# Kernel optimization log

Hardware: AMD Instinct MI355X
Metric: run time of the kernel (lower is better)

Reference implementation:

```python
import jax, jax.numpy as jnp
import numpy as np

N_NODE = 4095
D_EMB = 32
D_MODEL = 64
NHEADS = 8
ALPHA = 1.0
B = N_NODE + 1  # batch must equal n_node+1 (see einsum 'nm,tmd->tnd')
T = 32


def setup_inputs() -> dict:
    key = jax.random.key(0)
    ks = jax.random.split(key, 16)
    f32 = jnp.float32
    inp = {
        "q": jax.random.normal(ks[0], (B, T, D_MODEL), f32),
        "k": jax.random.normal(ks[1], (B, T, D_MODEL), f32),
        "v": jax.random.normal(ks[2], (B, T, D_MODEL), f32),
        # learned parameters (torch init is randn; scaled for numeric stability)
        "emb": jax.random.normal(ks[3], (N_NODE + 1, D_EMB), f32) * 0.05,
        "We": jax.random.normal(ks[4], (D_EMB, D_MODEL, D_MODEL), f32) * 0.05,
        "be": jax.random.normal(ks[5], (D_EMB, D_MODEL), f32) * 0.05,
        "Wq": jax.random.normal(ks[6], (D_MODEL, D_MODEL), f32) * 0.05,
        "bq": jax.random.normal(ks[7], (D_MODEL,), f32) * 0.05,
        "Wk": jax.random.normal(ks[8], (D_MODEL, D_MODEL), f32) * 0.05,
        "bk": jax.random.normal(ks[9], (D_MODEL,), f32) * 0.05,
        "Wv": jax.random.normal(ks[10], (D_MODEL, D_MODEL), f32) * 0.05,
        "bv": jax.random.normal(ks[11], (D_MODEL,), f32) * 0.05,
        "Wo": jax.random.normal(ks[12], (D_MODEL, D_MODEL), f32) * 0.05,
        "bo": jax.random.normal(ks[13], (D_MODEL,), f32) * 0.05,
    }
    return inp


def _elu(x, alpha):
    return jnp.where(x > 0, x, alpha * (jnp.exp(x) - 1.0))


def _split_heads(x, h):
    # torch.cat(torch.split(x, D//h, dim=-1), dim=0): [B,T,D] -> [h*B,T,D/h]
    b, t, d = x.shape
    return jnp.moveaxis(x.reshape(b, t, h, d // h), 2, 0).reshape(h * b, t, d // h)


def _merge_heads(x, b, h):
    # torch.cat(torch.split(x, B, dim=0), dim=-1): [h*B,T,D/h] -> [B,T,D]
    hb, t, dh = x.shape
    return jnp.moveaxis(x.reshape(h, b, t, dh), 0, 2).reshape(b, t, h * dh)


def reference(q, k, v, emb, We, be, Wq, bq, Wk, bk, Wv, bv, Wo, bo):
    Bq, Tq, D = q.shape
    h = NHEADS
    scale = (D // h) ** 0.5

    # linear projections (torch Linear: x @ W.T + b)
    q = q @ Wq.T + bq
    k = k @ Wk.T + bk
    v = v @ Wv.T + bv

    # adjacency: sum over d_emb of pairwise diff == s_i - s_j (same math, no [N,N,E] tensor)
    s = jnp.sum(emb, axis=-1)  # [N+1]
    sim = s[:, None] - s[None, :]  # [N+1, N+1]
    A = jax.nn.softmax(_elu(sim, ALPHA), axis=-1) + jnp.eye(Bq, dtype=q.dtype)

    # updateQ: adjacency-weighted diffusion + per-node weight matrices
    qt = jnp.transpose(q, (1, 0, 2))  # [T, N, D]
    W = jnp.einsum('ne,eio->nio', emb, We)  # [N, D, D]
    b = emb @ be  # [N, D]
    q_ = jnp.einsum('nm,tmd->tnd', A, qt)  # diffusion
    q_ = jnp.einsum('tnd,ndo->tno', q_, W) + b  # per-node matmul
    q = jnp.transpose(q_, (1, 0, 2))  # [N, T, D]

    # manual multi-head attention via split/cat
    qh = _split_heads(q, h)
    kh = _split_heads(k, h)
    vh = _split_heads(v, h)
    attn = jax.nn.softmax(jnp.einsum('btd,bsd->bts', qh, kh) / scale, axis=-1)
    out = jnp.einsum('bts,bsd->btd', attn, vh)
    out = _merge_heads(out, Bq, h)
    return out @ Wo.T + bo
```

## Files before the change

kernel.cpp:

```cpp
#include <hip/hip_runtime.h>
#include <hip/hip_bf16.h>

constexpr int NN  = 4096;
constexpr int DE  = 32;
constexpr int TD  = 2048;

typedef __attribute__((ext_vector_type(8))) short short8;
typedef __attribute__((ext_vector_type(4))) float f32x4;

#define MFMA16(a, b, c) __builtin_amdgcn_mfma_f32_16x16x32_bf16(a, b, c, 0, 0, 0)

__device__ inline ushort f2b(float x) {
    __hip_bfloat16 h = __float2bfloat16(x);
    union { __hip_bfloat16 h; ushort u; } c; c.h = h;
    return c.u;
}

__device__ inline float b2f(ushort u) {
    union { unsigned u; float f; } c; c.u = ((unsigned)u) << 16;
    return c.f;
}

__device__ inline short8 pack8(float4 a, float4 b) {
    short8 v;
    v[0] = (short)f2b(a.x); v[1] = (short)f2b(a.y); v[2] = (short)f2b(a.z); v[3] = (short)f2b(a.w);
    v[4] = (short)f2b(b.x); v[5] = (short)f2b(b.y); v[6] = (short)f2b(b.z); v[7] = (short)f2b(b.w);
    return v;
}

__device__ inline short8 pack8v(f32x4 a, f32x4 b) {
    short8 v;
    v[0] = (short)f2b(a[0]); v[1] = (short)f2b(a[1]); v[2] = (short)f2b(a[2]); v[3] = (short)f2b(a[3]);
    v[4] = (short)f2b(b[0]); v[5] = (short)f2b(b[1]); v[6] = (short)f2b(b[2]); v[7] = (short)f2b(b[3]);
    return v;
}

__device__ __forceinline__ short8 as_s8(f32x4 v) {
    union { f32x4 f; short8 s; } u; u.f = v; return u.s;
}

template<int OFF>
__device__ __forceinline__ f32x4 gl16(unsigned long long addr) {
    f32x4 d;
    asm volatile("global_load_dwordx4 %0, %1, off offset:%c2"
                 : "=v"(d) : "v"(addr), "n"(OFF) : "memory");
    return d;
}

template<int OFF>
__device__ __forceinline__ float gl4(unsigned long long addr) {
    float d;
    asm volatile("global_load_dword %0, %1, off offset:%c2"
                 : "=v"(d) : "v"(addr), "n"(OFF) : "memory");
    return d;
}

#define WAITV(N) asm volatile("s_waitcnt vmcnt(" #N ")" ::: "memory"); \
                 __builtin_amdgcn_sched_barrier(0)

__global__ __launch_bounds__(256) void k_prep(const float* __restrict__ emb,
                                              const float* __restrict__ We,
                                              const float* __restrict__ be,
                                              const float* __restrict__ Wk,
                                              const float* __restrict__ Wv,
                                              const float* __restrict__ Wo,
                                              float* __restrict__ s_g,
                                              ushort* __restrict__ embbf,
                                              ushort* __restrict__ WeTT,
                                              ushort* __restrict__ Wkbf,
                                              ushort* __restrict__ Wvbf,
                                              ushort* __restrict__ Wobf,
                                              float* __restrict__ bn) {
    int id = blockIdx.x, tid = threadIdx.x;
    if (id < 16) {
        int n = id * 256 + tid;
        const float4* e4 = (const float4*)(emb + n * DE);
        float s = 0.f;
#pragma unroll
        for (int i = 0; i < DE / 4; ++i) { float4 v = e4[i]; s += v.x + v.y + v.z + v.w; }
        s_g[n] = s;
    } else if (id < 144) {
        int g4 = (id - 16) * 256 + tid;
        float4 v = *(const float4*)&emb[(size_t)g4 * 4];
        ushort4 o; o.x = f2b(v.x); o.y = f2b(v.y); o.z = f2b(v.z); o.w = f2b(v.w);
        *(ushort4*)&embbf[(size_t)g4 * 4] = o;
    } else if (id < 176) {
        int e = id - 144;
#pragma unroll
        for (int u = 0; u < 4; ++u) {
            int idx0 = tid * 16 + u * 4;
            float4 v = *(const float4*)&We[(size_t)e * 4096 + idx0];
            float vv[4] = {v.x, v.y, v.z, v.w};
#pragma unroll
            for (int i = 0; i < 4; ++i) {
                int idx = idx0 + i;
                int o = idx & 63, d = idx >> 6;
                WeTT[(size_t)(o * 64 + d) * 32 + e] = f2b(vv[i]);
            }
        }
    } else if (id < 224) {
        int id5 = id - 176;
        int which = id5 >> 4, gid = (id5 & 15) * 256 + tid;
        const float* src = which == 0 ? Wk : (which == 1 ? Wv : Wo);
        ushort* dst = which == 0 ? Wkbf : (which == 1 ? Wvbf : Wobf);
        dst[gid] = f2b(src[gid]);
    } else {
        int gid = (id - 224) * 256 + tid;
        int n = gid >> 6, o = gid & 63;
        float acc = 0.f;
#pragma unroll
        for (int e = 0; e < DE; ++e) acc += emb[n * DE + e] * be[e * 64 + o];
        bn[gid] = acc;
    }
}

__global__ __launch_bounds__(256) void k_pr(const float* __restrict__ X,
                                            const float* __restrict__ W,
                                            const float* __restrict__ bias,
                                            ushort* __restrict__ Y,
                                            const float* __restrict__ s_g,
                                            int* __restrict__ perm) {
    __shared__ float ss[NN];
    int id = blockIdx.x, tid = threadIdx.x;
    if (id < 512) {
        int lane = tid & 63, wid = tid >> 6;
        int r0 = id * 256 + wid * 64;
        int l15 = lane & 15, kb = lane >> 4;
        f32x4 acc[4][4] = {};
#pragma unroll
        for (int kk = 0; kk < 2; ++kk) {
            short8 af[4], bf[4];
#pragma unroll
            for (int f = 0; f < 4; ++f) {
                const float* ap = X + (size_t)(r0 + f * 16 + l15) * 64 + kk * 32 + kb * 8;
                af[f] = pack8(*(const float4*)ap, *(const float4*)(ap + 4));
                const float* bp = W + (size_t)(f * 16 + l15) * 64 + kk * 32 + kb * 8;
                bf[f] = pack8(*(const float4*)bp, *(const float4*)(bp + 4));
            }
#pragma unroll
            for (int i = 0; i < 4; ++i)
#pragma unroll
                for (int j = 0; j < 4; ++j)
                    acc[i][j] = MFMA16(af[i], bf[j], acc[i][j]);
        }
        float bcol[4];
#pragma unroll
        for (int j = 0; j < 4; ++j) bcol[j] = bias[j * 16 + l15];
#pragma unroll
        for (int i = 0; i < 4; ++i)
#pragma unroll
            for (int j = 0; j < 4; ++j)
#pragma unroll
                for (int r = 0; r < 4; ++r)
                    Y[(size_t)(r0 + i * 16 + kb * 4 + r) * 64 + j * 16 + l15] =
                        f2b(acc[i][j][r] + bcol[j]);
    } else {
        for (int i = tid; i < NN; i += 256) ss[i] = s_g[i];
        __syncthreads();
        int g = tid >> 5, l = tid & 31;
        int n = (id - 512) * 8 + g;
        float sn = ss[n];
        int cnt = 0;
        for (int j2 = 0; j2 < 128; ++j2) {
            int m = j2 * 32 + l;
            float sm = ss[m];
            cnt += (sm < sn) || (sm == sn && m < n);
        }
        for (int off = 16; off; off >>= 1) cnt += __shfl_down(cnt, off, 32);
        if (l == 0) perm[cnt] = n;
    }
}

__global__ __launch_bounds__(256) void k_csum(const ushort* __restrict__ qp,
                                              const float* __restrict__ s_g,
                                              const int* __restrict__ perm,
                                              float* __restrict__ Cj,
                                              float* __restrict__ Cb) {
    __shared__ int ns[64];
    __shared__ float bs[64];
    int bx = blockIdx.x, by = blockIdx.y, tid = threadIdx.x;
    if (tid < 64) {
        int n = perm[bx * 64 + tid];
        ns[tid] = n;
        bs[tid] = __expf(-s_g[n]);
    }
    __syncthreads();
    int j = by * 256 + tid;
    float run[8] = {};
    for (int ii = 0; ii < 64; ++ii) {
        float qv = b2f(qp[(size_t)ns[ii] * 2048 + j]);
        float b = bs[ii], t = qv;
#pragma unroll
        for (int k2 = 0; k2 < 8; ++k2) { run[k2] += t; t *= b; }
    }
    float* cp = Cj + ((size_t)bx * 2048 + j) * 8;
    *(float4*)cp       = make_float4(run[0], run[1], run[2], run[3]);
    *(float4*)(cp + 4) = make_float4(run[4], run[5], run[6], run[7]);
    if (by == 0 && tid < 64) {
        float b = bs[tid], bk = 1.f;
#pragma unroll
        for (int k2 = 0; k2 < 8; ++k2) {
            float v = bk;
            for (int off = 32; off; off >>= 1) v += __shfl_down(v, off, 64);
            if (tid == 0) Cb[bx * 8 + k2] = v;
            bk *= b;
        }
    }
}

__global__ __launch_bounds__(256) void k_pre(const float* __restrict__ Cj,
                                             float* __restrict__ PRE,
                                             const float* __restrict__ Cb,
                                             float* __restrict__ CbPre) {
    __shared__ float sCb[512];
    int tid = threadIdx.x;
    if (blockIdx.x < 64) {
        int gid = blockIdx.x * 256 + tid;
        float run = 0.f;
#pragma unroll 8
        for (int c = 0; c < 64; ++c) {
            PRE[(size_t)c * 16384 + gid] = run;
            run += Cj[(size_t)c * 16384 + gid];
        }
        PRE[(size_t)64 * 16384 + gid] = run;
    } else {
        sCb[tid] = Cb[tid];
        sCb[tid + 256] = Cb[tid + 256];
        __syncthreads();
        if (tid < 8) {
            float run = 0.f;
            for (int c = 0; c < 64; ++c) {
                CbPre[c * 8 + tid] = run;
                run += sCb[c * 8 + tid];
            }
            CbPre[512 + tid] = run;
        }
    }
}

__global__ __launch_bounds__(256) void k_combw(const ushort* __restrict__ qp,
                                               const float* __restrict__ s_g,
                                               const int* __restrict__ perm,
                                               const float* __restrict__ PRE,
                                               const float* __restrict__ CbPre,
                                               ushort* __restrict__ qdifb,
                                               const ushort* __restrict__ embbf,
                                               const ushort* __restrict__ WeTT,
                                               ushort* __restrict__ WnT) {
    __shared__ int ns[64];
    __shared__ float sa[64], sb[64];
    int id = blockIdx.x, tid = threadIdx.x;
    if (id < 512) {
        int bx = id & 63, by = id >> 6;
        if (tid < 64) {
            int n = perm[bx * 64 + tid];
            ns[tid] = n;
            float s = s_g[n];
            sa[tid] = __expf(s);
            sb[tid] = __expf(-s);
        }
        __syncthreads();
        int j = by * 256 + tid;
        float T[8], pre[8];
        {
            const float* pp = PRE + (size_t)bx * 16384 + (size_t)j * 8;
            float4 u0 = *(const float4*)pp, u1 = *(const float4*)(pp + 4);
            pre[0] = u0.x; pre[1] = u0.y; pre[2] = u0.z; pre[3] = u0.w;
            pre[4] = u1.x; pre[5] = u1.y; pre[6] = u1.z; pre[7] = u1.w;
            const float* tp = PRE + (size_t)64 * 16384 + (size_t)j * 8;
            float4 t0 = *(const float4*)tp, t1 = *(const float4*)(tp + 4);
            T[0] = t0.x; T[1] = t0.y; T[2] = t0.z; T[3] = t0.w;
            T[4] = t1.x; T[5] = t1.y; T[6] = t1.z; T[7] = t1.w;
        }
        float TB[8], preb[8];
        {
            float4 v0 = *(const float4*)&CbPre[bx * 8], v1 = *(const float4*)&CbPre[bx * 8 + 4];
            preb[0] = v0.x; preb[1] = v0.y; preb[2] = v0.z; preb[3] = v0.w;
            preb[4] = v1.x; preb[5] = v1.y; preb[6] = v1.z; preb[7] = v1.w;
            float4 t0 = *(const float4*)&CbPre[512], t1 = *(const float4*)&CbPre[516];
            TB[0] = t0.x; TB[1] = t0.y; TB[2] = t0.z; TB[3] = t0.w;
            TB[4] = t1.x; TB[5] = t1.y; TB[6] = t1.z; TB[7] = t1.w;
        }
#pragma unroll 2
        for (int ii = 0; ii < 64; ++ii) {
            int n = ns[ii];
            float a = sa[ii], b = sb[ii];
            float g0 = 0.36787944117144233f;
            float g1 = g0 * a;
            float g2 = g1 * a * 0.5f;
            float g3 = g2 * a * (1.f / 3.f);
            float g4 = g3 * a * 0.25f;
            float g5 = g4 * a * 0.2f;
            float g6 = g5 * a * (1.f / 6.f);
            float g7 = g6 * a * (1.f / 7.f);
            float Z = a * preb[1]
                    + g0 * (TB[0] - preb[0]) + g1 * (TB[1] - preb[1])
                    + g2 * (TB[2] - preb[2]) + g3 * (TB[3] - preb[3])
                    + g4 * (TB[4] - preb[4]) + g5 * (TB[5] - preb[5])
                    + g6 * (TB[6] - preb[6]) + g7 * (TB[7] - preb[7]);
            float izv = 1.f / Z;
            float qv = b2f(qp[(size_t)n * 2048 + j]);
            float ss2 = g0 * (T[0] - pre[0]) + g1 * (T[1] - pre[1])
                      + g2 * (T[2] - pre[2]) + g3 * (T[3] - pre[3])
                      + g4 * (T[4] - pre[4]) + g5 * (T[5] - pre[5])
                      + g6 * (T[6] - pre[6]) + g7 * (T[7] - pre[7]);
            float outv = (a * pre[1] + ss2) * izv + qv;
            qdifb[(size_t)n * 2048 + j] = f2b(outv);
            float bk = 1.f;
#pragma unroll
            for (int k2 = 0; k2 < 8; ++k2) { pre[k2] += bk * qv; preb[k2] += bk; bk *= b; }
        }
    } else {
        int w2 = id - 512;
        int lane = tid & 63, wid = tid >> 6;
        int n0  = (w2 & 31) * 128 + (wid >> 1) * 64;
        int od0 = (w2 >> 5) * 128 + (wid & 1) * 64;
        int l15 = lane & 15, kb = lane >> 4;
        short8 af[4], bf[4];
#pragma unroll
        for (int f = 0; f < 4; ++f) {
            af[f] = *(const short8*)(embbf + (size_t)(n0 + f * 16 + l15) * 32 + kb * 8);
            bf[f] = *(const short8*)(WeTT + (size_t)(od0 + f * 16 + l15) * 32 + kb * 8);
        }
        f32x4 acc[4][4] = {};
#pragma unroll
        for (int i = 0; i < 4; ++i)
#pragma unroll
            for (int j = 0; j < 4; ++j)
                acc[i][j] = MFMA16(af[i], bf[j], acc[i][j]);
#pragma unroll
        for (int i = 0; i < 4; ++i)
#pragma unroll
            for (int j = 0; j < 4; ++j)
#pragma unroll
                for (int r = 0; r < 4; ++r)
                    WnT[(size_t)(n0 + i * 16 + kb * 4 + r) * 4096 + od0 + j * 16 + l15] =
                        f2b(acc[i][j][r]);
    }
}

__global__ __launch_bounds__(256, 2) void k_fused(const float* __restrict__ kin,
                                                  const float* __restrict__ vin,
                                                  const ushort* __restrict__ qdifb,
                                                  const ushort* __restrict__ WnT,
                                                  const float* __restrict__ bn,
                                                  const ushort* __restrict__ Wkbf,
                                                  const float* __restrict__ bk,
                                                  const ushort* __restrict__ Wvbf,
                                                  const float* __restrict__ bv,
                                                  const ushort* __restrict__ Wobf,
                                                  const float* __restrict__ bo,
                                                  float* __restrict__ out) {
    __shared__ ushort Kb[2176];
    __shared__ ushort Qb[2176];
    __shared__ ushort Vb[2560];
    __shared__ ushort Pb[4][1280];
    __shared__ ushort attb[2304];
    int tid = threadIdx.x, lane = tid & 63, w = tid >> 6;
    int b = blockIdx.x;
    int l15 = lane & 15, g = lane >> 4;
    int hh_w = l15 >> 3, d1_w = l15 & 7;
    const float SCALE = 0.35355339059327373f;
    short8 zfrag = {};

    f32x4 wx0, wx1, wx2, wx3, wx4, wx5, wx6, wx7;
    f32x4 x0, x1, x2, x3, x4, x5, x6, x7;
    float bxc0, bxc1, bxc2, bxc3;
    f32x4 q0v, q1v, q2v, q3v;
    f32x4 wn0, wn1, wn2, wn3;
    float bnc0, bnc1;
    f32x4 wo0, wo1; float boc;

    if (w < 2) {
        const float*  xin = w ? vin : kin;
        const ushort* Wx  = w ? Wvbf : Wkbf;
        const float*  bx_ = w ? bv : bk;
        unsigned long long bxA = (unsigned long long)(bx_ + l15);
        unsigned long long wxA = (unsigned long long)((const char*)Wx + l15 * 128 + g * 16 + 3072);
        unsigned long long xaA = (unsigned long long)(xin + (size_t)b * TD + (8 + l15) * 64 + g * 8);
        bxc0 = gl4<0>(bxA); bxc1 = gl4<64>(bxA); bxc2 = gl4<128>(bxA); bxc3 = gl4<192>(bxA);
        wx0 = gl16<-3072>(wxA); wx1 = gl16<-3008>(wxA);
        wx2 = gl16<-1024>(wxA); wx3 = gl16< -960>(wxA);
        wx4 = gl16< 1024>(wxA); wx5 = gl16< 1088>(wxA);
        wx6 = gl16< 3072>(wxA); wx7 = gl16< 3136>(wxA);
        x0 = gl16<-2048>(xaA); x1 = gl16<-2032>(xaA);
        x2 = gl16<-1920>(xaA); x3 = gl16<-1904>(xaA);
        x4 = gl16< 2048>(xaA); x5 = gl16< 2064>(xaA);
        x6 = gl16< 2176>(xaA); x7 = gl16< 2192>(xaA);
    } else {
        int wq = w - 2;
        unsigned long long qaA = (unsigned long long)(qdifb + (size_t)b * TD + (8 + l15) * 64 + g * 8);
        unsigned long long wnA = (unsigned long long)((const char*)(WnT + (size_t)b * 4096)
                                                      + ((size_t)(wq * 32 + l15)) * 128 + g * 16);
        unsigned long long bnA = (unsigned long long)(bn + (size_t)b * 64 + wq * 32 + l15);
        q0v = gl16<-1024>(qaA); q1v = gl16<-960>(qaA);
        q2v = gl16< 1024>(qaA); q3v = gl16<1088>(qaA);
        wn0 = gl16<0>(wnA); wn1 = gl16<64>(wnA);
        wn2 = gl16<2048>(wnA); wn3 = gl16<2112>(wnA);
        bnc0 = gl4<0>(bnA); bnc1 = gl4<64>(bnA);
    }
    {
        unsigned long long woA = (unsigned long long)((const char*)Wobf
                                                      + ((size_t)(w * 16 + l15)) * 128 + g * 16);
        unsigned long long boA = (unsigned long long)(bo + w * 16 + l15);
        wo0 = gl16<0>(woA); wo1 = gl16<64>(woA);
        boc = gl4<0>(boA);
    }

    if (w < 2) {
        WAITV(3);
        short8 xaf[2][2], wxf[4][2];
        xaf[0][0] = pack8v(x0, x1); xaf[1][0] = pack8v(x2, x3);
        xaf[0][1] = pack8v(x4, x5); xaf[1][1] = pack8v(x6, x7);
        wxf[0][0] = as_s8(wx0); wxf[0][1] = as_s8(wx1);
        wxf[1][0] = as_s8(wx2); wxf[1][1] = as_s8(wx3);
        wxf[2][0] = as_s8(wx4); wxf[2][1] = as_s8(wx5);
        wxf[3][0] = as_s8(wx6); wxf[3][1] = as_s8(wx7);
        float bxc[4] = {bxc0, bxc1, bxc2, bxc3};
#pragma unroll
        for (int j = 0; j < 4; ++j) {
            f32x4 ax[2] = {};
#pragma unroll
            for (int kk = 0; kk < 2; ++kk)
#pragma unroll
                for (int ti = 0; ti < 2; ++ti)
                    ax[ti] = MFMA16(xaf[kk][ti], wxf[j][kk], ax[ti]);
            if (w == 0) {
#pragma unroll
                for (int ti = 0; ti < 2; ++ti)
#pragma unroll
                    for (int r = 0; r < 4; ++r) {
                        int s = ti * 16 + g * 4 + r;
                        Kb[(j * 2 + hh_w) * 272 + s * 8 + d1_w] = f2b(ax[ti][r] + bxc[j]);
                    }
            } else {
#pragma unroll
                for (int ti = 0; ti < 2; ++ti)
#pragma unroll
                    for (int r = 0; r < 4; r += 2) {
                        int s = ti * 16 + g * 4 + r;
                        ushort2 p; p.x = f2b(ax[ti][r] + bxc[j]); p.y = f2b(ax[ti][r + 1] + bxc[j]);
                        *(ushort2*)&Vb[(j * 2 + hh_w) * 320 + d1_w * 40 + s] = p;
                    }
            }
        }
    } else {
        int wq = w - 2;
        WAITV(3);
        short8 qaf[2][2], wnf[2][2];
        qaf[0][0] = as_s8(q0v); qaf[1][0] = as_s8(q1v);
        qaf[0][1] = as_s8(q2v); qaf[1][1] = as_s8(q3v);
        wnf[0][0] = as_s8(wn0); wnf[0][1] = as_s8(wn1);
        wnf[1][0] = as_s8(wn2); wnf[1][1] = as_s8(wn3);
        float bnc[2] = {bnc0, bnc1};
#pragma unroll
        for (int jj = 0; jj < 2; ++jj) {
            int j = 2 * wq + jj;
            f32x4 aq[2] = {};
#pragma unroll
            for (int kk = 0; kk < 2; ++kk)
#pragma unroll
                for (int ti = 0; ti < 2; ++ti)
                    aq[ti] = MFMA16(qaf[kk][ti], wnf[jj][kk], aq[ti]);
#pragma unroll
            for (int ti = 0; ti < 2; ++ti)
#pragma unroll
                for (int r = 0; r < 4; ++r) {
                    int s = ti * 16 + g * 4 + r;
                    Qb[(j * 2 + hh_w) * 272 + s * 8 + d1_w] = f2b(aq[ti][r] + bnc[jj]);
                }
        }
    }
    __syncthreads();

#pragma unroll
    for (int hh = 0; hh < 2; ++hh) {
        int h = 2 * w + hh;
        short8 kf[2], qf[2];
#pragma unroll
        for (int si = 0; si < 2; ++si)
            kf[si] = (lane < 16) ? *(const short8*)&Kb[h * 272 + (si * 16 + l15) * 8] : zfrag;
#pragma unroll
        for (int ti = 0; ti < 2; ++ti)
            qf[ti] = (lane < 16) ? *(const short8*)&Qb[h * 272 + (ti * 16 + l15) * 8] : zfrag;
        f32x4 sc[2][2];
#pragma unroll
        for (int si = 0; si < 2; ++si)
#pragma unroll
            for (int ti = 0; ti < 2; ++ti)
                sc[si][ti] = MFMA16(kf[si], qf[ti], f32x4{});
#pragma unroll
        for (int ti = 0; ti < 2; ++ti) {
            float e0[4], e1[4], sm = 0.f;
#pragma unroll
            for (int r = 0; r < 4; ++r) {
                e0[r] = __expf(sc[0][ti][r] * SCALE);
                e1[r] = __expf(sc[1][ti][r] * SCALE);
                sm += e0[r] + e1[r];
            }
            sm += __shfl_xor(sm, 16);
            sm += __shfl_xor(sm, 32);
            float inv = 1.f / sm;
            int t = ti * 16 + l15;
            unsigned p00 = (unsigned)f2b(e0[0] * inv) | ((unsigned)f2b(e0[1] * inv) << 16);
            unsigned p01 = (unsigned)f2b(e0[2] * inv) | ((unsigned)f2b(e0[3] * inv) << 16);
            unsigned p10 = (unsigned)f2b(e1[0] * inv) | ((unsigned)f2b(e1[1] * inv) << 16);
            unsigned p11 = (unsigned)f2b(e1[2] * inv) | ((unsigned)f2b(e1[3] * inv) << 16);
            *(unsigned*)&Pb[w][t * 40 + g * 4]          = p00;
            *(unsigned*)&Pb[w][t * 40 + g * 4 + 2]      = p01;
            *(unsigned*)&Pb[w][t * 40 + 16 + g * 4]     = p10;
            *(unsigned*)&Pb[w][t * 40 + 16 + g * 4 + 2] = p11;
        }
        short8 vf = *(const short8*)&Vb[h * 320 + (l15 & 7) * 40 + g * 8];
#pragma unroll
        for (int ti = 0; ti < 2; ++ti) {
            short8 af = *(const short8*)&Pb[w][(ti * 16 + l15) * 40 + g * 8];
            f32x4 pv = MFMA16(af, vf, f32x4{});
            if (l15 < 8) {
#pragma unroll
                for (int r = 0; r < 4; ++r)
                    attb[(ti * 16 + g * 4 + r) * 72 + h * 8 + l15] = f2b(pv[r]);
            }
        }
    }
    __syncthreads();

    WAITV(0);
    {
        short8 wof[2];
        wof[0] = as_s8(wo0); wof[1] = as_s8(wo1);
        short8 aof[2][2];
#pragma unroll
        for (int kk = 0; kk < 2; ++kk)
#pragma unroll
            for (int ti = 0; ti < 2; ++ti)
                aof[kk][ti] = *(const short8*)&attb[(ti * 16 + l15) * 72 + kk * 32 + g * 8];
        f32x4 co[2] = {};
#pragma unroll
        for (int kk = 0; kk < 2; ++kk)
#pragma unroll
            for (int ti = 0; ti < 2; ++ti)
                co[ti] = MFMA16(aof[kk][ti], wof[kk], co[ti]);
#pragma unroll
        for (int ti = 0; ti < 2; ++ti)
#pragma unroll
            for (int r = 0; r < 4; ++r)
                out[(size_t)b * TD + (ti * 16 + g * 4 + r) * 64 + w * 16 + l15] =
                    co[ti][r] + boc;
    }
}

extern "C" void kernel_launch(void* const* d_in, const int* in_sizes, int n_in,
                              void* d_out, int out_size, void* d_ws, size_t ws_size,
                              hipStream_t stream) {
    const float* q   = (const float*)d_in[0];
    const float* k   = (const float*)d_in[1];
    const float* v   = (const float*)d_in[2];
    const float* emb = (const float*)d_in[3];
    const float* We  = (const float*)d_in[4];
    const float* be  = (const float*)d_in[5];
    const float* Wq  = (const float*)d_in[6];
    const float* bq  = (const float*)d_in[7];
    const float* Wk  = (const float*)d_in[8];
    const float* bk  = (const float*)d_in[9];
    const float* Wv  = (const float*)d_in[10];
    const float* bv  = (const float*)d_in[11];
    const float* Wo  = (const float*)d_in[12];
    const float* bo  = (const float*)d_in[13];

    float* ws = (float*)d_ws;
    ushort* qp    = (ushort*)ws;
    ushort* WnT   = (ushort*)(ws + 4194304);
    ushort* qdifb = (ushort*)(ws + 12582912);
    float*  Cj    = ws + 16777216;
    float*  bn    = ws + 17825792;
    float*  s_g   = ws + 18087936;
    int*    perm  = (int*)(ws + 18092032);
    float*  Cb    = ws + 18096128;
    ushort* embbf = (ushort*)(ws + 18096640);
    ushort* WeTT  = (ushort*)(ws + 18162176);
    ushort* Wkbf  = (ushort*)(ws + 18227712);
    ushort* Wvbf  = (ushort*)(ws + 18229760);
    ushort* Wobf  = (ushort*)(ws + 18231808);
    float*  PRE   = ws + 18233856;
    float*  CbPre = ws + 19298816;
    float*  outp  = (float*)d_out;

    k_prep <<<1248, 256, 0, stream>>>(emb, We, be, Wk, Wv, Wo,
                                      s_g, embbf, WeTT, Wkbf, Wvbf, Wobf, bn);
    k_pr   <<<1024, 256, 0, stream>>>(q, Wq, bq, qp, s_g, perm);
    k_csum <<<dim3(64, 8), 256, 0, stream>>>(qp, s_g, perm, Cj, Cb);
    k_pre  <<<65, 256, 0, stream>>>(Cj, PRE, Cb, CbPre);
    k_combw<<<1536, 256, 0, stream>>>(qp, s_g, perm, PRE, CbPre, qdifb,
                                      embbf, WeTT, WnT);
    k_fused<<<4096, 256, 0, stream>>>(k, v, qdifb, WnT, bn,
                                      Wkbf, bk, Wvbf, bv, Wobf, bo, outp);
}
```

Before: 107.0 us.

## Process two nodes per block in fused attention kernel, prefetching second node's inputs

```diff
diff --git a/kernel.cpp b/kernel.cpp
--- a/kernel.cpp
+++ b/kernel.cpp
@@ -357,7 +357,7 @@
     __shared__ ushort Pb[4][1280];
     __shared__ ushort attb[2304];
     int tid = threadIdx.x, lane = tid & 63, w = tid >> 6;
-    int b = blockIdx.x;
+    int b0 = blockIdx.x * 2;
     int l15 = lane & 15, g = lane >> 4;
     int hh_w = l15 >> 3, d1_w = l15 & 7;
     const float SCALE = 0.35355339059327373f;
@@ -365,10 +365,11 @@
 
     f32x4 wx0, wx1, wx2, wx3, wx4, wx5, wx6, wx7;
     f32x4 x0, x1, x2, x3, x4, x5, x6, x7;
+    f32x4 y0, y1, y2, y3, y4, y5, y6, y7;
     float bxc0, bxc1, bxc2, bxc3;
-    f32x4 q0v, q1v, q2v, q3v;
-    f32x4 wn0, wn1, wn2, wn3;
-    float bnc0, bnc1;
+    f32x4 q0v, q1v, q2v, q3v, wn0, wn1, wn2, wn3;
+    f32x4 r0v, r1v, r2v, r3v, um0, um1, um2, um3;
+    float bn0c0, bn0c1, bn1c0, bn1c1;
     f32x4 wo0, wo1; float boc;
 
     if (w < 2) {
@@ -377,7 +378,8 @@
         const float*  bx_ = w ? bv : bk;
         unsigned long long bxA = (unsigned long long)(bx_ + l15);
         unsigned long long wxA = (unsigned long long)((const char*)Wx + l15 * 128 + g * 16 + 3072);
-        unsigned long long xaA = (unsigned long long)(xin + (size_t)b * TD + (8 + l15) * 64 + g * 8);
+        unsigned long long xaA = (unsigned long long)(xin + (size_t)b0 * TD + (8 + l15) * 64 + g * 8);
+        unsigned long long yaA = (unsigned long long)(xin + (size_t)(b0 + 1) * TD + (8 + l15) * 64 + g * 8);
         bxc0 = gl4<0>(bxA); bxc1 = gl4<64>(bxA); bxc2 = gl4<128>(bxA); bxc3 = gl4<192>(bxA);
         wx0 = gl16<-3072>(wxA); wx1 = gl16<-3008>(wxA);
         wx2 = gl16<-1024>(wxA); wx3 = gl16< -960>(wxA);
@@ -387,31 +389,49 @@
         x2 = gl16<-1920>(xaA); x3 = gl16<-1904>(xaA);
         x4 = gl16< 2048>(xaA); x5 = gl16< 2064>(xaA);
         x6 = gl16< 2176>(xaA); x7 = gl16< 2192>(xaA);
+        {
+            unsigned long long woA = (unsigned long long)((const char*)Wobf
+                                                          + ((size_t)(w * 16 + l15)) * 128 + g * 16);
+            unsigned long long boA = (unsigned long long)(bo + w * 16 + l15);
+            wo0 = gl16<0>(woA); wo1 = gl16<64>(woA);
+            boc = gl4<0>(boA);
+        }
+        y0 = gl16<-2048>(yaA); y1 = gl16<-2032>(yaA);
+        y2 = gl16<-1920>(yaA); y3 = gl16<-1904>(yaA);
+        y4 = gl16< 2048>(yaA); y5 = gl16< 2064>(yaA);
+        y6 = gl16< 2176>(yaA); y7 = gl16< 2192>(yaA);
     } else {
         int wq = w - 2;
-        unsigned long long qaA = (unsigned long long)(qdifb + (size_t)b * TD + (8 + l15) * 64 + g * 8);
-        unsigned long long wnA = (unsigned long long)((const char*)(WnT + (size_t)b * 4096)
+        unsigned long long qaA = (unsigned long long)(qdifb + (size_t)b0 * TD + (8 + l15) * 64 + g * 8);
+        unsigned long long wnA = (unsigned long long)((const char*)(WnT + (size_t)b0 * 4096)
                                                       + ((size_t)(wq * 32 + l15)) * 128 + g * 16);
-        unsigned long long bnA = (unsigned long long)(bn + (size_t)b * 64 + wq * 32 + l15);
+        unsigned long long bnA = (unsigned long long)(bn + (size_t)b0 * 64 + wq * 32 + l15);
+        unsigned long long qbA = (unsigned long long)(qdifb + (size_t)(b0 + 1) * TD + (8 + l15) * 64 + g * 8);
+        unsigned long long wmA = (unsigned long long)((const char*)(WnT + (size_t)(b0 + 1) * 4096)
+                                                      + ((size_t)(wq * 32 + l15)) * 128 + g * 16);
+        unsigned long long bmA = (unsigned long long)(bn + (size_t)(b0 + 1) * 64 + wq * 32 + l15);
         q0v = gl16<-1024>(qaA); q1v = gl16<-960>(qaA);
         q2v = gl16< 1024>(qaA); q3v = gl16<1088>(qaA);
         wn0 = gl16<0>(wnA); wn1 = gl16<64>(wnA);
         wn2 = gl16<2048>(wnA); wn3 = gl16<2112>(wnA);
-        bnc0 = gl4<0>(bnA); bnc1 = gl4<64>(bnA);
-    }
-    {
-        unsigned long long woA = (unsigned long long)((const char*)Wobf
-                                                      + ((size_t)(w * 16 + l15)) * 128 + g * 16);
-        unsigned long long boA = (unsigned long long)(bo + w * 16 + l15);
-        wo0 = gl16<0>(woA); wo1 = gl16<64>(woA);
-        boc = gl4<0>(boA);
-    }
-
-    if (w < 2) {
-        WAITV(3);
-        short8 xaf[2][2], wxf[4][2];
-        xaf[0][0] = pack8v(x0, x1); xaf[1][0] = pack8v(x2, x3);
-        xaf[0][1] = pack8v(x4, x5); xaf[1][1] = pack8v(x6, x7);
+        bn0c0 = gl4<0>(bnA); bn0c1 = gl4<64>(bnA);
+        {
+            unsigned long long woA = (unsigned long long)((const char*)Wobf
+                                                          + ((size_t)(w * 16 + l15)) * 128 + g * 16);
+            unsigned long long boA = (unsigned long long)(bo + w * 16 + l15);
+            wo0 = gl16<0>(woA); wo1 = gl16<64>(woA);
+            boc = gl4<0>(boA);
+        }
+        r0v = gl16<-1024>(qbA); r1v = gl16<-960>(qbA);
+        r2v = gl16< 1024>(qbA); r3v = gl16<1088>(qbA);
+        um0 = gl16<0>(wmA); um1 = gl16<64>(wmA);
+        um2 = gl16<2048>(wmA); um3 = gl16<2112>(wmA);
+        bn1c0 = gl4<0>(bmA); bn1c1 = gl4<64>(bmA);
+    }
+
+    auto kvProj = [&](short8 xaf00, short8 xaf10, short8 xaf01, short8 xaf11) {
+        short8 xaf[2][2] = {{xaf00, xaf01}, {xaf10, xaf11}};
+        short8 wxf[4][2];
         wxf[0][0] = as_s8(wx0); wxf[0][1] = as_s8(wx1);
         wxf[1][0] = as_s8(wx2); wxf[1][1] = as_s8(wx3);
         wxf[2][0] = as_s8(wx4); wxf[2][1] = as_s8(wx5);
@@ -444,15 +464,14 @@
                     }
             }
         }
-    } else {
+    };
+    auto qProj = [&](short8 qa00, short8 qa10, short8 qa01, short8 qa11,
+                     short8 wf00, short8 wf01, short8 wf10, short8 wf11,
+                     float bc0, float bc1) {
+        short8 qaf[2][2] = {{qa00, qa01}, {qa10, qa11}};
+        short8 wnf[2][2] = {{wf00, wf01}, {wf10, wf11}};
+        float bnc[2] = {bc0, bc1};
         int wq = w - 2;
-        WAITV(3);
-        short8 qaf[2][2], wnf[2][2];
-        qaf[0][0] = as_s8(q0v); qaf[1][0] = as_s8(q1v);
-        qaf[0][1] = as_s8(q2v); qaf[1][1] = as_s8(q3v);
-        wnf[0][0] = as_s8(wn0); wnf[0][1] = as_s8(wn1);
-        wnf[1][0] = as_s8(wn2); wnf[1][1] = as_s8(wn3);
-        float bnc[2] = {bnc0, bnc1};
 #pragma unroll
         for (int jj = 0; jj < 2; ++jj) {
             int j = 2 * wq + jj;
@@ -470,63 +489,60 @@
                     Qb[(j * 2 + hh_w) * 272 + s * 8 + d1_w] = f2b(aq[ti][r] + bnc[jj]);
                 }
         }
-    }
-    __syncthreads();
-
-#pragma unroll
-    for (int hh = 0; hh < 2; ++hh) {
-        int h = 2 * w + hh;
-        short8 kf[2], qf[2];
-#pragma unroll
-        for (int si = 0; si < 2; ++si)
-            kf[si] = (lane < 16) ? *(const short8*)&Kb[h * 272 + (si * 16 + l15) * 8] : zfrag;
-#pragma unroll
-        for (int ti = 0; ti < 2; ++ti)
-            qf[ti] = (lane < 16) ? *(const short8*)&Qb[h * 272 + (ti * 16 + l15) * 8] : zfrag;
-        f32x4 sc[2][2];
-#pragma unroll
-        for (int si = 0; si < 2; ++si)
+    };
+    auto attn = [&]() {
+#pragma unroll
+        for (int hh = 0; hh < 2; ++hh) {
+            int h = 2 * w + hh;
+            short8 kf[2], qf[2];
+#pragma unroll
+            for (int si = 0; si < 2; ++si)
+                kf[si] = (lane < 16) ? *(const short8*)&Kb[h * 272 + (si * 16 + l15) * 8] : zfrag;
 #pragma unroll
             for (int ti = 0; ti < 2; ++ti)
-                sc[si][ti] = MFMA16(kf[si], qf[ti], f32x4{});
-#pragma unroll
-        for (int ti = 0; ti < 2; ++ti) {
-            float e0[4], e1[4], sm = 0.f;
-#pragma unroll
-            for (int r = 0; r < 4; ++r) {
-                e0[r] = __expf(sc[0][ti][r] * SCALE);
-                e1[r] = __expf(sc[1][ti][r] * SCALE);
-                sm += e0[r] + e1[r];
+                qf[ti] = (lane < 16) ? *(const short8*)&Qb[h * 272 + (ti * 16 + l15) * 8] : zfrag;
+            f32x4 sc[2][2];
+#pragma unroll
+            for (int si = 0; si < 2; ++si)
+#pragma unroll
+                for (int ti = 0; ti < 2; ++ti)
+                    sc[si][ti] = MFMA16(kf[si], qf[ti], f32x4{});
+#pragma unroll
+            for (int ti = 0; ti < 2; ++ti) {
+                float e0[4], e1[4], sm = 0.f;
+#pragma unroll
+                for (int r = 0; r < 4; ++r) {
+                    e0[r] = __expf(sc[0][ti][r] * SCALE);
+                    e1[r] = __expf(sc[1][ti][r] * SCALE);
+                    sm += e0[r] + e1[r];
+                }
+                sm += __shfl_xor(sm, 16);
+                sm += __shfl_xor(sm, 32);
+                float inv = 1.f / sm;
+                int t = ti * 16 + l15;
+                unsigned p00 = (unsigned)f2b(e0[0] * inv) | ((unsigned)f2b(e0[1] * inv) << 16);
+                unsigned p01 = (unsigned)f2b(e0[2] * inv) | ((unsigned)f2b(e0[3] * inv) << 16);
+                unsigned p10 = (unsigned)f2b(e1[0] * inv) | ((unsigned)f2b(e1[1] * inv) << 16);
+                unsigned p11 = (unsigned)f2b(e1[2] * inv) | ((unsigned)f2b(e1[3] * inv) << 16);
+                *(unsigned*)&Pb[w][t * 40 + g * 4]          = p00;
+                *(unsigned*)&Pb[w][t * 40 + g * 4 + 2]      = p01;
+                *(unsigned*)&Pb[w][t * 40 + 16 + g * 4]     = p10;
+                *(unsigned*)&Pb[w][t * 40 + 16 + g * 4 + 2] = p11;
             }
-            sm += __shfl_xor(sm, 16);
-            sm += __shfl_xor(sm, 32);
-            float inv = 1.f / sm;
-            int t = ti * 16 + l15;
-            unsigned p00 = (unsigned)f2b(e0[0] * inv) | ((unsigned)f2b(e0[1] * inv) << 16);
-            unsigned p01 = (unsigned)f2b(e0[2] * inv) | ((unsigned)f2b(e0[3] * inv) << 16);
-            unsigned p10 = (unsigned)f2b(e1[0] * inv) | ((unsigned)f2b(e1[1] * inv) << 16);
-            unsigned p11 = (unsigned)f2b(e1[2] * inv) | ((unsigned)f2b(e1[3] * inv) << 16);
-            *(unsigned*)&Pb[w][t * 40 + g * 4]          = p00;
-            *(unsigned*)&Pb[w][t * 40 + g * 4 + 2]      = p01;
-            *(unsigned*)&Pb[w][t * 40 + 16 + g * 4]     = p10;
-            *(unsigned*)&Pb[w][t * 40 + 16 + g * 4 + 2] = p11;
-        }
-        short8 vf = *(const short8*)&Vb[h * 320 + (l15 & 7) * 40 + g * 8];
-#pragma unroll
-        for (int ti = 0; ti < 2; ++ti) {
-            short8 af = *(const short8*)&Pb[w][(ti * 16 + l15) * 40 + g * 8];
-            f32x4 pv = MFMA16(af, vf, f32x4{});
-            if (l15 < 8) {
-#pragma unroll
-                for (int r = 0; r < 4; ++r)
-                    attb[(ti * 16 + g * 4 + r) * 72 + h * 8 + l15] = f2b(pv[r]);
+            short8 vf = *(const short8*)&Vb[h * 320 + (l15 & 7) * 40 + g * 8];
+#pragma unroll
+            for (int ti = 0; ti < 2; ++ti) {
+                short8 af = *(const short8*)&Pb[w][(ti * 16 + l15) * 40 + g * 8];
+                f32x4 pv = MFMA16(af, vf, f32x4{});
+                if (l15 < 8) {
+#pragma unroll
+                    for (int r = 0; r < 4; ++r)
+                        attb[(ti * 16 + g * 4 + r) * 72 + h * 8 + l15] = f2b(pv[r]);
+                }
             }
         }
-    }
-    __syncthreads();
-
-    WAITV(0);
-    {
+    };
+    auto epi = [&](int bb) {
         short8 wof[2];
         wof[0] = as_s8(wo0); wof[1] = as_s8(wo1);
         short8 aof[2][2];
@@ -545,9 +561,34 @@
         for (int ti = 0; ti < 2; ++ti)
 #pragma unroll
             for (int r = 0; r < 4; ++r)
-                out[(size_t)b * TD + (ti * 16 + g * 4 + r) * 64 + w * 16 + l15] =
+                out[(size_t)bb * TD + (ti * 16 + g * 4 + r) * 64 + w * 16 + l15] =
                     co[ti][r] + boc;
-    }
+    };
+
+    if (w < 2) {
+        WAITV(11);
+        kvProj(pack8v(x0, x1), pack8v(x2, x3), pack8v(x4, x5), pack8v(x6, x7));
+    } else {
+        WAITV(13);
+        qProj(as_s8(q0v), as_s8(q1v), as_s8(q2v), as_s8(q3v),
+              as_s8(wn0), as_s8(wn1), as_s8(wn2), as_s8(wn3), bn0c0, bn0c1);
+    }
+    __syncthreads();
+    attn();
+    __syncthreads();
+    WAITV(8);
+    epi(b0);
+    WAITV(0);
+    if (w < 2) {
+        kvProj(pack8v(y0, y1), pack8v(y2, y3), pack8v(y4, y5), pack8v(y6, y7));
+    } else {
+        qProj(as_s8(r0v), as_s8(r1v), as_s8(r2v), as_s8(r3v),
+              as_s8(um0), as_s8(um1), as_s8(um2), as_s8(um3), bn1c0, bn1c1);
+    }
+    __syncthreads();
+    attn();
+    __syncthreads();
+    epi(b0 + 1);
 }
 
 extern "C" void kernel_launch(void* const* d_in, const int* in_sizes, int n_in,
@@ -593,6 +634,6 @@
     k_pre  <<<65, 256, 0, stream>>>(Cj, PRE, Cb, CbPre);
     k_combw<<<1536, 256, 0, stream>>>(qp, s_g, perm, PRE, CbPre, qdifb,
                                       embbf, WeTT, WnT);
-    k_fused<<<4096, 256, 0, stream>>>(k, v, qdifb, WnT, bn,
+    k_fused<<<2048, 256, 0, stream>>>(k, v, qdifb, WnT, bn,
                                       Wkbf, bk, Wvbf, bv, Wobf, bo, outp);
 }
```

Measured after the change: 114.3 us. 1.07x slower.
